# Performance work log

Measured on AMD Instinct MI355X. Metric: run time of the kernel, lower is better.

The kernel has to match this reference:

```python
import jax, jax.numpy as jnp
import numpy as np

K = 6            # kmer length
NF = 8192        # n_filters (> 4**K so kmer_params has shape (NF, 4, K))
M = 4 ** K       # 4096 kmers
B = 1024         # batch


def setup_inputs() -> dict:
    key = jax.random.key(0)
    k1, k2 = jax.random.split(key)
    freq = jax.random.uniform(k1, (B, M), dtype=jnp.float32)          # kmer frequencies (B, 4^k)
    kmer_params = jax.random.normal(k2, (NF, 4, K), dtype=jnp.float32)
    temperature = jnp.ones((1,), dtype=jnp.float32)
    # base-4 digits of arange(4^k), most-significant first == itertools.product order
    pos = 4 ** jnp.arange(K - 1, -1, -1)
    kmer_idcs = ((jnp.arange(M)[:, None] // pos[None, :]) % 4).astype(jnp.int32)  # (M, K)
    return {"freq": freq, "kmer_params": kmer_params,
            "temperature": temperature, "kmer_idcs": kmer_idcs}


def reference(freq, kmer_params, temperature, kmer_idcs):
    k = kmer_params.shape[-1]
    # matches[f, i] = sum_j kmer_params[f, kmer_idcs[i, j], j]
    # Advanced indexing broadcasts (M, k) indices against arange(k): result (F, M, k).
    # This replaces torch's expand-to-(F, M, 1, k) + gather + squeeze + sum(-1).
    matches = kmer_params[:, kmer_idcs, jnp.arange(k)].sum(axis=-1)   # (F, M)
    probs = jax.nn.softmax(matches / temperature, axis=1)             # softmax over kmers
    pooled = freq @ probs.T                                           # (B, F)
    profile = pooled / pooled.sum(axis=1, keepdims=True)
    return profile
```

## Files before the change

kernel.cpp:

```cpp
#include <hip/hip_runtime.h>


typedef __bf16  bf16x8 __attribute__((ext_vector_type(8)));
typedef float   f32x4  __attribute__((ext_vector_type(4)));

#define GLD16(gp, lp)                                                          \
  __builtin_amdgcn_global_load_lds(                                            \
      (const __attribute__((address_space(1))) void*)(gp),                     \
      (__attribute__((address_space(3))) void*)(lp), 16, 0, 0)

__device__ __forceinline__ short f2bf(float x) {
  unsigned u = __float_as_uint(x);
  unsigned r = (u + 0x7fffu + ((u >> 16) & 1u)) >> 16;
  return (short)r;
}

__device__ __forceinline__ float wave_max(float v) {
  #pragma unroll
  for (int off = 32; off; off >>= 1) v = fmaxf(v, __shfl_xor(v, off, 64));
  return v;
}
__device__ __forceinline__ float wave_sum(float v) {
  #pragma unroll
  for (int off = 32; off; off >>= 1) v += __shfl_xor(v, off, 64);
  return v;
}

__global__ __launch_bounds__(256) void cast_kernel(const float* __restrict__ in,
                                                   short* __restrict__ out) {
  int idx = blockIdx.x * 256 + threadIdx.x;
  float4 v = ((const float4*)in)[idx];
  short4 o;
  o.x = f2bf(v.x); o.y = f2bf(v.y); o.z = f2bf(v.z); o.w = f2bf(v.w);
  ((short4*)out)[idx] = o;
}

__global__ __launch_bounds__(256) void tables_kernel(const float* __restrict__ kp,
                                                     const float* __restrict__ temp,
                                                     float* __restrict__ E1t,
                                                     float* __restrict__ E2) {
  const int t = threadIdx.x;
  const int lane = t & 63, wave = t >> 6;
  const int f = blockIdx.x * 4 + wave;
  const float* P = kp + f * 24;
  const int d0 = (lane >> 4) & 3, d1 = (lane >> 2) & 3, d2 = lane & 3;
  const float thi = P[d0 * 6 + 0] + P[d1 * 6 + 1] + P[d2 * 6 + 2];
  const float tlo = P[d0 * 6 + 3] + P[d1 * 6 + 4] + P[d2 * 6 + 5];
  const float mxhi = wave_max(thi), mxlo = wave_max(tlo);
  const float invT = 1.0f / temp[0];
  const float e1 = __expf((thi - mxhi) * invT);
  const float e2 = __expf((tlo - mxlo) * invT);
  const float s1 = wave_sum(e1), s2 = wave_sum(e2);
  const float invZ = 1.0f / (s1 * s2);
  E1t[lane * 8192 + f] = e1 * invZ;
  E2[(size_t)f * 64 + lane] = e2;
}

__global__ __launch_bounds__(256, 4) void gemm_kernel(const short* __restrict__ A,
                                                      const float* __restrict__ E1t,
                                                      const float* __restrict__ E2,
                                                      float* __restrict__ C) {
  __shared__ short As[3][64 * 64];

  const int t = threadIdx.x;
  const int lane = t & 63, wave = t >> 6;
  const int quad = lane >> 4, l16 = lane & 15;

  const int d  = blockIdx.y * 64 + blockIdx.x;
  const int L  = (d & 7) * 128 + (d >> 3);
  const int m0 = (L >> 6) * 64;
  const int n0 = (L & 63) * 128;
  const int wn = wave * 32;

  f32x4 acc[4][2];
  #pragma unroll
  for (int i = 0; i < 4; i++)
    #pragma unroll
    for (int j = 0; j < 2; j++) acc[i][j] = (f32x4){0.f, 0.f, 0.f, 0.f};

  int nrow[2];
  #pragma unroll
  for (int j = 0; j < 2; j++) nrow[j] = n0 + wn + j * 16 + l16;
  bf16x8 e2f[2][2];
  #pragma unroll
  for (int j = 0; j < 2; j++)
    #pragma unroll
    for (int ks = 0; ks < 2; ks++) {
      const float* p = E2 + (size_t)nrow[j] * 64 + (ks * 4 + quad) * 8;
      float4 lo = *(const float4*)p, hi = *(const float4*)(p + 4);
      bf16x8 bb;
      bb[0] = (__bf16)lo.x; bb[1] = (__bf16)lo.y;
      bb[2] = (__bf16)lo.z; bb[3] = (__bf16)lo.w;
      bb[4] = (__bf16)hi.x; bb[5] = (__bf16)hi.y;
      bb[6] = (__bf16)hi.z; bb[7] = (__bf16)hi.w;
      e2f[ks][j] = bb;
    }

  const int lane_row = lane >> 3;
  const int src_col = ((lane & 7) ^ lane_row) * 8;
  const int sw = l16 & 7;
  const int chunk = wave * 2;
  const short* Abase = A + (size_t)(m0 + lane_row) * 4096 + src_col;

  #define STG(kt, buf) do {                                                    \
    GLD16(Abase + (size_t)((chunk + 0) * 8) * 4096 + (kt) * 64,                \
          &As[buf][(chunk + 0) * 512 + lane * 8]);                             \
    GLD16(Abase + (size_t)((chunk + 1) * 8) * 4096 + (kt) * 64,                \
          &As[buf][(chunk + 1) * 512 + lane * 8]);                             \
  } while (0)

  STG(0, 0);
  float e1n[2], e1c[2];
  #pragma unroll
  for (int j = 0; j < 2; j++) e1n[j] = E1t[nrow[j]];
  STG(1, 1);

  const f32x4 Z4 = (f32x4){0.f, 0.f, 0.f, 0.f};

  #pragma unroll 1
  for (int kt = 0; kt < 64; ++kt) {
    const int cb = kt % 3;
    const int sb = (kt + 2) % 3;
    const int tn = (kt + 1 > 63) ? 63 : kt + 1;
    const int ts = (kt + 2 > 63) ? 63 : kt + 2;

    asm volatile("s_waitcnt vmcnt(4)" ::: "memory");
    __builtin_amdgcn_s_barrier();

    bf16x8 a[4][2];
    #pragma unroll
    for (int i = 0; i < 4; i++)
      #pragma unroll
      for (int ks = 0; ks < 2; ks++)
        a[i][ks] = *(const bf16x8*)&As[cb][(i * 16 + l16) * 64 +
                                          (((ks * 4 + quad) ^ sw) * 8)];

    #pragma unroll
    for (int j = 0; j < 2; j++) e1c[j] = e1n[j];
    #pragma unroll
    for (int j = 0; j < 2; j++) e1n[j] = E1t[tn * 8192 + nrow[j]];
    STG(ts, sb);

    __builtin_amdgcn_s_setprio(1);
    #pragma unroll
    for (int j = 0; j < 2; j++) {
      const f32x4 s4 = (f32x4){e1c[j], e1c[j], e1c[j], e1c[j]};
      #pragma unroll
      for (int i = 0; i < 4; i++) {
        f32x4 P = __builtin_amdgcn_mfma_f32_16x16x32_bf16(a[i][0], e2f[0][j], Z4, 0, 0, 0);
        P = __builtin_amdgcn_mfma_f32_16x16x32_bf16(a[i][1], e2f[1][j], P, 0, 0, 0);
        acc[i][j] += s4 * P;
      }
    }
    __builtin_amdgcn_s_setprio(0);
  }

  asm volatile("s_waitcnt vmcnt(0)" ::: "memory");

  #pragma unroll
  for (int i = 0; i < 4; i++) {
    #pragma unroll
    for (int r = 0; r < 4; r++) {
      const int brow = m0 + i * 16 + quad * 4 + r;
      float* crow = C + (size_t)brow * 8192 + n0 + wn + l16;
      #pragma unroll
      for (int j = 0; j < 2; j++) crow[j * 16] = acc[i][j][r];
    }
  }
  #undef STG
}

__global__ __launch_bounds__(256) void norm_kernel(float* __restrict__ out) {
  const int b = blockIdx.x;
  const int t = threadIdx.x;
  const int lane = t & 63, wave = t >> 6;
  __shared__ float red[4];

  float4* row = (float4*)(out + (size_t)b * 8192);
  float4 v[8];
  float s = 0.0f;
  #pragma unroll
  for (int q = 0; q < 8; q++) {
    v[q] = row[q * 256 + t];
    s += (v[q].x + v[q].y) + (v[q].z + v[q].w);
  }
  float ws = wave_sum(s);
  if (lane == 0) red[wave] = ws;
  __syncthreads();
  float tot = (red[0] + red[1]) + (red[2] + red[3]);
  float inv = 1.0f / tot;
  #pragma unroll
  for (int q = 0; q < 8; q++) {
    v[q].x *= inv; v[q].y *= inv; v[q].z *= inv; v[q].w *= inv;
    row[q * 256 + t] = v[q];
  }
}

extern "C" void kernel_launch(void* const* d_in, const int* in_sizes, int n_in,
                              void* d_out, int out_size, void* d_ws, size_t ws_size,
                              hipStream_t stream) {
  const float* freq    = (const float*)d_in[0];
  const float* kparams = (const float*)d_in[1];
  const float* temp    = (const float*)d_in[2];

  float* out = (float*)d_out;

  short* freqb = (short*)d_ws;
  float* E1t   = (float*)(freqb + (size_t)1024 * 4096);
  float* E2    = E1t + (size_t)64 * 8192;

  cast_kernel  <<<4096, 256, 0, stream>>>(freq, freqb);
  tables_kernel<<<2048, 256, 0, stream>>>(kparams, temp, E1t, E2);
  gemm_kernel  <<<dim3(64, 16), 256, 0, stream>>>(freqb, E1t, E2, out);
  norm_kernel  <<<1024, 256, 0, stream>>>(out);
}
```

Before: 157.9 us.

## Fuse row normalization into GEMM via atomic row sums and grid barrier

Measured after the change: 275.2 us. 74.3% more time.

```diff
diff --git a/kernel.cpp b/kernel.cpp
--- a/kernel.cpp
+++ b/kernel.cpp
@@ -9,6 +9,8 @@
       (const __attribute__((address_space(1))) void*)(gp),                     \
       (__attribute__((address_space(3))) void*)(lp), 16, 0, 0)
 
+#define NBLK 1024
+
 __device__ __forceinline__ short f2bf(float x) {
   unsigned u = __float_as_uint(x);
   unsigned r = (u + 0x7fffu + ((u >> 16) & 1u)) >> 16;
@@ -26,40 +28,49 @@
   return v;
 }
 
-__global__ __launch_bounds__(256) void cast_kernel(const float* __restrict__ in,
-                                                   short* __restrict__ out) {
-  int idx = blockIdx.x * 256 + threadIdx.x;
-  float4 v = ((const float4*)in)[idx];
-  short4 o;
-  o.x = f2bf(v.x); o.y = f2bf(v.y); o.z = f2bf(v.z); o.w = f2bf(v.w);
-  ((short4*)out)[idx] = o;
-}
-
-__global__ __launch_bounds__(256) void tables_kernel(const float* __restrict__ kp,
-                                                     const float* __restrict__ temp,
-                                                     float* __restrict__ E1t,
-                                                     float* __restrict__ E2) {
-  const int t = threadIdx.x;
-  const int lane = t & 63, wave = t >> 6;
-  const int f = blockIdx.x * 4 + wave;
-  const float* P = kp + f * 24;
-  const int d0 = (lane >> 4) & 3, d1 = (lane >> 2) & 3, d2 = lane & 3;
-  const float thi = P[d0 * 6 + 0] + P[d1 * 6 + 1] + P[d2 * 6 + 2];
-  const float tlo = P[d0 * 6 + 3] + P[d1 * 6 + 4] + P[d2 * 6 + 5];
-  const float mxhi = wave_max(thi), mxlo = wave_max(tlo);
-  const float invT = 1.0f / temp[0];
-  const float e1 = __expf((thi - mxhi) * invT);
-  const float e2 = __expf((tlo - mxlo) * invT);
-  const float s1 = wave_sum(e1), s2 = wave_sum(e2);
-  const float invZ = 1.0f / (s1 * s2);
-  E1t[lane * 8192 + f] = e1 * invZ;
-  E2[(size_t)f * 64 + lane] = e2;
+__global__ __launch_bounds__(256) void prep_kernel(const float* __restrict__ freq,
+                                                   short* __restrict__ freqb,
+                                                   const float* __restrict__ kp,
+                                                   const float* __restrict__ temp,
+                                                   float* __restrict__ E1t,
+                                                   float* __restrict__ E2,
+                                                   float* __restrict__ rowsum,
+                                                   int* __restrict__ cnt) {
+  if (blockIdx.x < 4096) {
+    int idx = blockIdx.x * 256 + threadIdx.x;
+    float4 v = ((const float4*)freq)[idx];
+    short4 o;
+    o.x = f2bf(v.x); o.y = f2bf(v.y); o.z = f2bf(v.z); o.w = f2bf(v.w);
+    ((short4*)freqb)[idx] = o;
+    if (blockIdx.x == 0) {
+      ((float4*)rowsum)[threadIdx.x] = (float4){0.f, 0.f, 0.f, 0.f};
+      if (threadIdx.x == 0) *cnt = 0;
+    }
+  } else {
+    const int t = threadIdx.x;
+    const int lane = t & 63, wave = t >> 6;
+    const int f = (blockIdx.x - 4096) * 4 + wave;
+    const float* P = kp + f * 24;
+    const int d0 = (lane >> 4) & 3, d1 = (lane >> 2) & 3, d2 = lane & 3;
+    const float thi = P[d0 * 6 + 0] + P[d1 * 6 + 1] + P[d2 * 6 + 2];
+    const float tlo = P[d0 * 6 + 3] + P[d1 * 6 + 4] + P[d2 * 6 + 5];
+    const float mxhi = wave_max(thi), mxlo = wave_max(tlo);
+    const float invT = 1.0f / temp[0];
+    const float e1 = __expf((thi - mxhi) * invT);
+    const float e2 = __expf((tlo - mxlo) * invT);
+    const float s1 = wave_sum(e1), s2 = wave_sum(e2);
+    const float invZ = 1.0f / (s1 * s2);
+    E1t[lane * 8192 + f] = e1 * invZ;
+    E2[(size_t)f * 64 + lane] = e2;
+  }
 }
 
 __global__ __launch_bounds__(256, 4) void gemm_kernel(const short* __restrict__ A,
                                                       const float* __restrict__ E1t,
                                                       const float* __restrict__ E2,
-                                                      float* __restrict__ C) {
+                                                      float* __restrict__ C,
+                                                      float* __restrict__ rowsum,
+                                                      int* __restrict__ cnt) {
   __shared__ short As[3][64 * 64];
 
   const int t = threadIdx.x;
@@ -157,43 +168,45 @@
 
   asm volatile("s_waitcnt vmcnt(0)" ::: "memory");
 
+  float rs[4][4];
+  #pragma unroll
+  for (int i = 0; i < 4; i++)
+    #pragma unroll
+    for (int r = 0; r < 4; r++) {
+      float p = acc[i][0][r] + acc[i][1][r];
+      #pragma unroll
+      for (int off = 1; off < 16; off <<= 1) p += __shfl_xor(p, off, 64);
+      rs[i][r] = p;
+    }
+  if (l16 == 0) {
+    #pragma unroll
+    for (int i = 0; i < 4; i++)
+      #pragma unroll
+      for (int r = 0; r < 4; r++)
+        atomicAdd(&rowsum[m0 + i * 16 + quad * 4 + r], rs[i][r]);
+  }
+
+  __syncthreads();
+  if (t == 0) {
+    atomicAdd(cnt, 1);
+    while (__hip_atomic_load(cnt, __ATOMIC_RELAXED, __HIP_MEMORY_SCOPE_AGENT) < NBLK)
+      __builtin_amdgcn_s_sleep(8);
+  }
+  __syncthreads();
+  __threadfence();
+
   #pragma unroll
   for (int i = 0; i < 4; i++) {
     #pragma unroll
     for (int r = 0; r < 4; r++) {
       const int brow = m0 + i * 16 + quad * 4 + r;
+      const float inv = 1.0f / rowsum[brow];
       float* crow = C + (size_t)brow * 8192 + n0 + wn + l16;
       #pragma unroll
-      for (int j = 0; j < 2; j++) crow[j * 16] = acc[i][j][r];
+      for (int j = 0; j < 2; j++) crow[j * 16] = acc[i][j][r] * inv;
     }
   }
   #undef STG
-}
-
-__global__ __launch_bounds__(256) void norm_kernel(float* __restrict__ out) {
-  const int b = blockIdx.x;
-  const int t = threadIdx.x;
-  const int lane = t & 63, wave = t >> 6;
-  __shared__ float red[4];
-
-  float4* row = (float4*)(out + (size_t)b * 8192);
-  float4 v[8];
-  float s = 0.0f;
-  #pragma unroll
-  for (int q = 0; q < 8; q++) {
-    v[q] = row[q * 256 + t];
-    s += (v[q].x + v[q].y) + (v[q].z + v[q].w);
-  }
-  float ws = wave_sum(s);
-  if (lane == 0) red[wave] = ws;
-  __syncthreads();
-  float tot = (red[0] + red[1]) + (red[2] + red[3]);
-  float inv = 1.0f / tot;
-  #pragma unroll
-  for (int q = 0; q < 8; q++) {
-    v[q].x *= inv; v[q].y *= inv; v[q].z *= inv; v[q].w *= inv;
-    row[q * 256 + t] = v[q];
-  }
 }
 
 extern "C" void kernel_launch(void* const* d_in, const int* in_sizes, int n_in,
@@ -205,12 +218,13 @@
 
   float* out = (float*)d_out;
 
-  short* freqb = (short*)d_ws;
-  float* E1t   = (float*)(freqb + (size_t)1024 * 4096);
-  float* E2    = E1t + (size_t)64 * 8192;
-
-  cast_kernel  <<<4096, 256, 0, stream>>>(freq, freqb);
-  tables_kernel<<<2048, 256, 0, stream>>>(kparams, temp, E1t, E2);
-  gemm_kernel  <<<dim3(64, 16), 256, 0, stream>>>(freqb, E1t, E2, out);
-  norm_kernel  <<<1024, 256, 0, stream>>>(out);
-}
+  short* freqb  = (short*)d_ws;
+  float* E1t    = (float*)(freqb + (size_t)1024 * 4096);
+  float* E2     = E1t + (size_t)64 * 8192;
+  float* rowsum = E2 + (size_t)8192 * 64;
+  int*   cnt    = (int*)(rowsum + 1024);
+
+  prep_kernel<<<6144, 256, 0, stream>>>(freq, freqb, kparams, temp, E1t, E2,
+                                        rowsum, cnt);
+  gemm_kernel<<<dim3(64, 16), 256, 0, stream>>>(freqb, E1t, E2, out, rowsum, cnt);
+}
```
